# Kernel optimization log

Measured on AMD Instinct MI355X. Metric: run time of the kernel, lower is better.

The kernel has to match this reference:

```python
import jax, jax.numpy as jnp
import numpy as np

EPS_LN = 1e-5
EPS_STD = 1e-5


def _ln_dim1(z, g, b):
    # LayerNorm over channel dim (axis=1) of (B, C, T) or (B, C, 1)
    mu = z.mean(axis=1, keepdims=True)
    var = ((z - mu) ** 2).mean(axis=1, keepdims=True)
    return (z - mu) * jax.lax.rsqrt(var + EPS_LN) * g[None, :, None] + b[None, :, None]


def _stats(x, m):
    # weighted mean/std over time axis; m broadcasts over channels
    mean = (m * x).sum(axis=2)                                   # (B, C)
    std = jnp.sqrt(jnp.maximum((m * x * x).sum(axis=2) - mean ** 2, EPS_STD))
    return mean, std


def setup_inputs() -> dict:
    key = jax.random.key(0)
    ks = jax.random.split(key, 4)
    B, C, T, H = 16, 1536, 2000, 128
    x = jax.random.normal(ks[0], (B, C, T), dtype=jnp.float32)
    mask = jnp.ones((B, 1, T), dtype=jnp.float32)
    # attention MLP params (conv1x1 -> relu -> LN(dim=1) -> tanh -> conv1x1)
    w1 = jax.random.normal(ks[1], (H, 3 * C), dtype=jnp.float32) * (1.0 / np.sqrt(3 * C))
    b1 = jnp.zeros((H,), jnp.float32)
    g1 = jnp.ones((H,), jnp.float32)
    be1 = jnp.zeros((H,), jnp.float32)
    w2 = jax.random.normal(ks[2], (C, H), dtype=jnp.float32) * (1.0 / np.sqrt(H))
    b2 = jnp.zeros((C,), jnp.float32)
    g2 = jnp.ones((2 * C,), jnp.float32)
    be2 = jnp.zeros((2 * C,), jnp.float32)
    return {"x": x, "mask": mask, "w1": w1, "b1": b1, "g1": g1, "be1": be1,
            "w2": w2, "b2": b2, "g2": g2, "be2": be2}


def reference(x, mask, w1, b1, g1, be1, w2, b2, g2, be2):
    B, C, T = x.shape
    # time_attention: append masked global mean/std, broadcast over T
    total = mask.sum(axis=2, keepdims=True)                      # (B,1,1)
    mean0, std0 = _stats(x, mask / total)                        # (B,C)
    x_in = jnp.concatenate([
        x,
        jnp.broadcast_to(mean0[:, :, None], (B, C, T)),
        jnp.broadcast_to(std0[:, :, None], (B, C, T)),
    ], axis=1)                                                   # (B,3C,T)
    # attention MLP (conv1x1 == channel matmul)
    h = jnp.einsum("hc,bct->bht", w1, x_in) + b1[None, :, None]  # (B,H,T)
    h = jnp.tanh(_ln_dim1(jax.nn.relu(h), g1, be1))
    alpha = jnp.einsum("ch,bht->bct", w2, h) + b2[None, :, None]  # (B,C,T)
    # masked softmax over time
    alpha = jnp.where(mask == 0, -jnp.inf, alpha)
    alpha = jax.nn.softmax(alpha, axis=2)
    # attention-weighted stats
    mean, std = _stats(x, alpha)                                 # (B,C) each
    out = jnp.concatenate([mean, std], axis=1)[:, :, None]       # (B,2C,1)
    return _ln_dim1(out, g2, be2)
```

## Files before the change

### kernel.cpp

```cpp
#include <hip/hip_runtime.h>
#include <math.h>

constexpr int B_  = 16;
constexpr int C_  = 1536;
constexpr int T_  = 2000;
constexpr int H_  = 128;
constexpr int C3_ = 3 * C_;
constexpr int C2_ = 2 * C_;
constexpr int NT_ = 4;

typedef short bf8 __attribute__((ext_vector_type(8)));
typedef short bf4 __attribute__((ext_vector_type(4)));
typedef float f4  __attribute__((ext_vector_type(4)));

__device__ inline unsigned short f2b(float f) {
  unsigned int u = __builtin_bit_cast(unsigned int, f);
  unsigned int r = (u + 0x7FFFu + ((u >> 16) & 1u)) >> 16;
  return (unsigned short)r;
}

__global__ __launch_bounds__(256) void k_stats(
    const float* __restrict__ x, const float* __restrict__ mask,
    float* __restrict__ mean0, float* __restrict__ std0) {
  const int wave = threadIdx.x >> 6;
  const int lane = threadIdx.x & 63;
  const int row = blockIdx.x * 4 + wave;
  const int b = row / C_;
  const float4* xr = (const float4*)(x + (size_t)row * T_);
  const float4* mr = (const float4*)(mask + (size_t)b * T_);
  float sm = 0.f, s1 = 0.f, s2 = 0.f;
  for (int i = lane; i < T_ / 4; i += 64) {
    float4 xv = xr[i];
    float4 mv = mr[i];
    sm += mv.x + mv.y + mv.z + mv.w;
    s1 += mv.x * xv.x + mv.y * xv.y + mv.z * xv.z + mv.w * xv.w;
    s2 += mv.x * xv.x * xv.x + mv.y * xv.y * xv.y + mv.z * xv.z * xv.z + mv.w * xv.w * xv.w;
  }
#pragma unroll
  for (int off = 32; off; off >>= 1) {
    sm += __shfl_xor(sm, off);
    s1 += __shfl_xor(s1, off);
    s2 += __shfl_xor(s2, off);
  }
  if (lane == 0) {
    float mean = s1 / sm;
    float var = s2 / sm - mean * mean;
    mean0[row] = mean;
    std0[row] = sqrtf(fmaxf(var, 1e-5f));
  }
}

__global__ __launch_bounds__(256) void k_hconst(
    const float* __restrict__ w1, const float* __restrict__ b1,
    const float* __restrict__ mean0, const float* __restrict__ std0,
    float* __restrict__ hconst) {
  const int wave = threadIdx.x >> 6;
  const int lane = threadIdx.x & 63;
  const int idx = blockIdx.x * 4 + wave;
  const int b = idx >> 7;
  const int h = idx & (H_ - 1);
  const float* wm  = w1 + (size_t)h * C3_ + C_;
  const float* wsd = wm + C_;
  const float* mn = mean0 + b * C_;
  const float* sd = std0 + b * C_;
  float s = 0.f;
  for (int c = lane; c < C_; c += 64)
    s += wm[c] * mn[c] + wsd[c] * sd[c];
#pragma unroll
  for (int off = 32; off; off >>= 1) s += __shfl_xor(s, off);
  if (lane == 0) hconst[idx] = s + b1[h];
}

__global__ __launch_bounds__(256) void k_wl1(
    const float* __restrict__ w2, float* __restrict__ wl1) {
  const int wave = threadIdx.x >> 6;
  const int lane = threadIdx.x & 63;
  const int c = blockIdx.x * 4 + wave;
  const float* wr = w2 + (size_t)c * H_;
  float s = fabsf(wr[lane]) + fabsf(wr[lane + 64]);
#pragma unroll
  for (int off = 32; off; off >>= 1) s += __shfl_xor(s, off);
  if (lane == 0) wl1[c] = s;
}

__global__ __launch_bounds__(256) void k_gemm1_ln(
    const float* __restrict__ x, const float* __restrict__ w1,
    const float* __restrict__ hconst, const float* __restrict__ g1,
    const float* __restrict__ be1, unsigned short* __restrict__ hlnT) {
  __shared__ __align__(16) short As[2][128 * 32];
  __shared__ __align__(16) short Bs[2][64 * 32];
  const int b = blockIdx.y;
  const int t0 = blockIdx.x * 64;
  const int tid = threadIdx.x;
  const int lane = tid & 63;
  const int w = tid >> 6;
  const int l15 = lane & 15;
  const int l4 = lane >> 4;

  float4 va[4], vb[2];

  f4 acc[8];
#pragma unroll
  for (int mi = 0; mi < 8; ++mi) { f4 z = {0.f, 0.f, 0.f, 0.f}; acc[mi] = z; }

#define G1_GLOAD(K0)                                                          \
  {                                                                           \
    _Pragma("unroll")                                                         \
    for (int q = 0; q < 4; ++q) {                                             \
      int idx = q * 256 + tid;                                                \
      int row = idx >> 3, j4 = idx & 7;                                       \
      va[q] = *(const float4*)(w1 + (size_t)row * C3_ + (K0) + j4 * 4);       \
    }                                                                         \
    _Pragma("unroll")                                                         \
    for (int q = 0; q < 2; ++q) {                                             \
      int idx = q * 256 + tid;                                                \
      int k = idx >> 4, t4 = idx & 15;                                        \
      int t = t0 + t4 * 4;                                                    \
      if (t < T_)                                                             \
        vb[q] = *(const float4*)(x + ((size_t)(b * C_ + (K0) + k)) * T_ + t); \
      else                                                                    \
        vb[q] = make_float4(0.f, 0.f, 0.f, 0.f);                              \
    }                                                                         \
  }
#define G1_LSTORE(BUF)                                                        \
  {                                                                           \
    _Pragma("unroll")                                                         \
    for (int q = 0; q < 4; ++q) {                                             \
      int idx = q * 256 + tid;                                                \
      int row = idx >> 3, j4 = idx & 7;                                       \
      int slot = (j4 >> 1) ^ ((row >> 2) & 3);                                \
      bf4 p;                                                                  \
      p[0] = (short)f2b(va[q].x); p[1] = (short)f2b(va[q].y);                 \
      p[2] = (short)f2b(va[q].z); p[3] = (short)f2b(va[q].w);                 \
      *(bf4*)&As[BUF][row * 32 + slot * 8 + (j4 & 1) * 4] = p;                \
    }                                                                         \
    _Pragma("unroll")                                                         \
    for (int q = 0; q < 2; ++q) {                                             \
      int idx = q * 256 + tid;                                                \
      int k = idx >> 4, t4 = idx & 15;                                        \
      float vv[4] = {vb[q].x, vb[q].y, vb[q].z, vb[q].w};                     \
      _Pragma("unroll")                                                       \
      for (int j = 0; j < 4; ++j) {                                           \
        int row = t4 * 4 + j;                                                 \
        int slot = (k >> 3) ^ ((row >> 2) & 3);                               \
        Bs[BUF][row * 32 + slot * 8 + (k & 7)] = (short)f2b(vv[j]);           \
      }                                                                       \
    }                                                                         \
  }

  G1_GLOAD(0);
  G1_LSTORE(0);
  __syncthreads();

  const int fA = (l15 >> 2) & 3;
  const int NS = C_ / 32;
  for (int s = 0; s < NS; ++s) {
    const int cur = s & 1;
    if (s + 1 < NS) G1_GLOAD((s + 1) * 32);
    {
      const int browB = w * 16 + l15;
      bf8 bfr = *(const bf8*)&Bs[cur][browB * 32 + (l4 ^ fA) * 8];
#pragma unroll
      for (int mi = 0; mi < 8; ++mi) {
        bf8 afr = *(const bf8*)&As[cur][(mi * 16 + l15) * 32 + (l4 ^ fA) * 8];
        acc[mi] = __builtin_amdgcn_mfma_f32_16x16x32_bf16(afr, bfr, acc[mi], 0, 0, 0);
      }
    }
    if (s + 1 < NS) G1_LSTORE(cur ^ 1);
    __syncthreads();
  }

  const int t = t0 + w * 16 + l15;
  float sum = 0.f, ssq = 0.f;
#pragma unroll
  for (int mi = 0; mi < 8; ++mi) {
    float4 h4 = *(const float4*)(hconst + b * H_ + mi * 16 + l4 * 4);
    const float* hp = (const float*)&h4;
#pragma unroll
    for (int reg = 0; reg < 4; ++reg) {
      float v = fmaxf(acc[mi][reg] + hp[reg], 0.f);
      acc[mi][reg] = v;
      sum += v;
      ssq += v * v;
    }
  }
  sum += __shfl_xor(sum, 16); sum += __shfl_xor(sum, 32);
  ssq += __shfl_xor(ssq, 16); ssq += __shfl_xor(ssq, 32);
  const float mean = sum * (1.f / 128.f);
  const float rstd = rsqrtf(ssq * (1.f / 128.f) - mean * mean + 1e-5f);
  if (t < T_) {
    unsigned short* dst = hlnT + ((size_t)b * T_ + t) * H_;
#pragma unroll
    for (int mi = 0; mi < 8; ++mi) {
      float4 g4 = *(const float4*)(g1 + mi * 16 + l4 * 4);
      float4 e4 = *(const float4*)(be1 + mi * 16 + l4 * 4);
      const float* gp = (const float*)&g4;
      const float* ep = (const float*)&e4;
      bf4 p;
#pragma unroll
      for (int reg = 0; reg < 4; ++reg) {
        float o = tanhf((acc[mi][reg] - mean) * rstd * gp[reg] + ep[reg]);
        p[reg] = (short)f2b(o);
      }
      *(bf4*)&dst[mi * 16 + l4 * 4] = p;
    }
  }
}

__global__ __launch_bounds__(256) void k_gemm2_pool(
    const float* __restrict__ x, const float* __restrict__ mask,
    const float* __restrict__ w2, const unsigned short* __restrict__ hlnT,
    const float* __restrict__ wl1,
    float* __restrict__ ps0, float* __restrict__ ps1, float* __restrict__ ps2) {
  __shared__ __align__(16) short Ws[128 * 128];
  __shared__ __align__(16) short Hs[2][64 * 128];
  const int b = blockIdx.y;
  const int c0 = blockIdx.x * 128;
  const int part = blockIdx.z;
  const int tb = part * 512;
  const int te = min(tb + 512, T_);
  const int tid = threadIdx.x;
  const int lane = tid & 63;
  const int w = tid >> 6;
  const int l15 = lane & 15;
  const int l4 = lane >> 4;

#pragma unroll
  for (int q = 0; q < 16; ++q) {
    int idx = q * 256 + tid;
    int row = idx >> 5, j4 = idx & 31;
    float4 v = *(const float4*)(w2 + (size_t)(c0 + row) * H_ + j4 * 4);
    bf4 p;
    p[0] = (short)f2b(v.x); p[1] = (short)f2b(v.y);
    p[2] = (short)f2b(v.z); p[3] = (short)f2b(v.w);
    int slot = (j4 >> 1) ^ (row & 15);
    *(bf4*)&Ws[row * 128 + slot * 8 + (j4 & 1) * 4] = p;
  }

  float Mc[8];
#pragma unroll
  for (int mi = 0; mi < 2; ++mi) {
    float4 m4 = *(const float4*)(wl1 + c0 + w * 32 + mi * 16 + l4 * 4);
    Mc[mi * 4 + 0] = m4.x; Mc[mi * 4 + 1] = m4.y;
    Mc[mi * 4 + 2] = m4.z; Mc[mi * 4 + 3] = m4.w;
  }

  float s0[8], s1[8], s2[8];
#pragma unroll
  for (int r = 0; r < 8; ++r) { s0[r] = 0.f; s1[r] = 0.f; s2[r] = 0.f; }

  bf8 hreg[4];
#define G2_HLOAD(T0)                                                          \
  {                                                                           \
    _Pragma("unroll")                                                         \
    for (int q = 0; q < 4; ++q) {                                             \
      int idx = q * 256 + tid;                                                \
      int row = idx >> 4, slot = idx & 15;                                    \
      int t = (T0) + row;                                                     \
      if (t > T_ - 1) t = T_ - 1;                                             \
      hreg[q] = *(const bf8*)(hlnT + ((size_t)b * T_ + t) * H_ + slot * 8);   \
    }                                                                         \
  }
#define G2_HSTORE(BUF)                                                        \
  {                                                                           \
    _Pragma("unroll")                                                         \
    for (int q = 0; q < 4; ++q) {                                             \
      int idx = q * 256 + tid;                                                \
      int row = idx >> 4, slot = idx & 15;                                    \
      *(bf8*)&Hs[BUF][row * 128 + (slot ^ (row & 15)) * 8] = hreg[q];         \
    }                                                                         \
  }

  G2_HLOAD(tb);
  G2_HSTORE(0);
  __syncthreads();

  const int NCH = (te - tb + 63) / 64;
  for (int ch = 0; ch < NCH; ++ch) {
    const int t0 = tb + ch * 64;
    const int cur = ch & 1;
    if (ch + 1 < NCH) G2_HLOAD(t0 + 64);

    float mk[4];
    int tcol[4];
#pragma unroll
    for (int nj = 0; nj < 4; ++nj) {
      int t = t0 + nj * 16 + l15;
      tcol[nj] = (t < T_) ? t : (T_ - 1);
      mk[nj] = (t < T_) ? mask[(size_t)b * T_ + t] : 0.f;
    }
    float xv[8][4];
#pragma unroll
    for (int mi = 0; mi < 2; ++mi)
#pragma unroll
      for (int reg = 0; reg < 4; ++reg) {
        const int c = c0 + w * 32 + mi * 16 + l4 * 4 + reg;
        const float* xrow = x + ((size_t)(b * C_ + c)) * T_;
#pragma unroll
        for (int nj = 0; nj < 4; ++nj) xv[mi * 4 + reg][nj] = xrow[tcol[nj]];
      }

    f4 acc[2][4];
#pragma unroll
    for (int mi = 0; mi < 2; ++mi)
#pragma unroll
      for (int nj = 0; nj < 4; ++nj) { f4 z = {0.f, 0.f, 0.f, 0.f}; acc[mi][nj] = z; }

#pragma unroll
    for (int ks = 0; ks < 4; ++ks) {
      const int sw = (ks * 4 + l4) ^ l15;
      bf8 a0 = *(const bf8*)&Ws[(w * 32 + l15) * 128 + sw * 8];
      bf8 a1 = *(const bf8*)&Ws[(w * 32 + 16 + l15) * 128 + sw * 8];
      bf8 bb[4];
#pragma unroll
      for (int nj = 0; nj < 4; ++nj)
        bb[nj] = *(const bf8*)&Hs[cur][(nj * 16 + l15) * 128 + sw * 8];
#pragma unroll
      for (int nj = 0; nj < 4; ++nj) {
        acc[0][nj] = __builtin_amdgcn_mfma_f32_16x16x32_bf16(a0, bb[nj], acc[0][nj], 0, 0, 0);
        acc[1][nj] = __builtin_amdgcn_mfma_f32_16x16x32_bf16(a1, bb[nj], acc[1][nj], 0, 0, 0);
      }
    }

#pragma unroll
    for (int mi = 0; mi < 2; ++mi)
#pragma unroll
      for (int reg = 0; reg < 4; ++reg) {
        const int r = mi * 4 + reg;
        float a0 = s0[r], a1 = s1[r], a2 = s2[r];
#pragma unroll
        for (int nj = 0; nj < 4; ++nj) {
          float e = (mk[nj] != 0.f) ? __expf(acc[mi][nj][reg] - Mc[r]) : 0.f;
          float xvv = xv[r][nj];
          a0 += e; a1 += e * xvv; a2 += e * xvv * xvv;
        }
        s0[r] = a0; s1[r] = a1; s2[r] = a2;
      }

    if (ch + 1 < NCH) G2_HSTORE(cur ^ 1);
    __syncthreads();
  }

#pragma unroll
  for (int off = 1; off < 16; off <<= 1) {
#pragma unroll
    for (int r = 0; r < 8; ++r) {
      s0[r] += __shfl_xor(s0[r], off);
      s1[r] += __shfl_xor(s1[r], off);
      s2[r] += __shfl_xor(s2[r], off);
    }
  }
  if (l15 == 0) {
#pragma unroll
    for (int mi = 0; mi < 2; ++mi)
#pragma unroll
      for (int reg = 0; reg < 4; ++reg) {
        const int r = mi * 4 + reg;
        const int c = c0 + w * 32 + mi * 16 + l4 * 4 + reg;
        const size_t j = ((size_t)(b * NT_ + part)) * C_ + c;
        ps0[j] = s0[r]; ps1[j] = s1[r]; ps2[j] = s2[r];
      }
  }
}

__global__ __launch_bounds__(256) void k_pool_merge(
    const float* __restrict__ ps0, const float* __restrict__ ps1,
    const float* __restrict__ ps2, float* __restrict__ pooled) {
  const int idx = blockIdx.x * 256 + threadIdx.x;
  const int b = idx / C_;
  const int c = idx - b * C_;
  float s0 = 0.f, s1 = 0.f, s2 = 0.f;
#pragma unroll
  for (int p = 0; p < NT_; ++p) {
    const size_t j = ((size_t)(b * NT_ + p)) * C_ + c;
    s0 += ps0[j]; s1 += ps1[j]; s2 += ps2[j];
  }
  float mean = s1 / s0;
  float var = s2 / s0 - mean * mean;
  pooled[b * C2_ + c] = mean;
  pooled[b * C2_ + C_ + c] = sqrtf(fmaxf(var, 1e-5f));
}

__global__ __launch_bounds__(256) void k_final_ln(
    const float* __restrict__ pooled, const float* __restrict__ g2,
    const float* __restrict__ be2, float* __restrict__ out) {
  __shared__ float rs[8];
  const int b = blockIdx.x;
  const int tid = threadIdx.x;
  const int lane = tid & 63;
  const int wave = tid >> 6;
  const float* p = pooled + b * C2_;
  float s = 0.f, q = 0.f;
  for (int i = tid; i < C2_; i += 256) {
    float v = p[i];
    s += v;
    q += v * v;
  }
#pragma unroll
  for (int off = 32; off; off >>= 1) {
    s += __shfl_xor(s, off);
    q += __shfl_xor(q, off);
  }
  if (lane == 0) { rs[wave] = s; rs[4 + wave] = q; }
  __syncthreads();
  s = rs[0] + rs[1] + rs[2] + rs[3];
  q = rs[4] + rs[5] + rs[6] + rs[7];
  float mean = s * (1.f / C2_);
  float var = q * (1.f / C2_) - mean * mean;
  float rstd = rsqrtf(var + 1e-5f);
  for (int i = tid; i < C2_; i += 256)
    out[b * C2_ + i] = (p[i] - mean) * rstd * g2[i] + be2[i];
}

extern "C" void kernel_launch(void* const* d_in, const int* in_sizes, int n_in,
                              void* d_out, int out_size, void* d_ws, size_t ws_size,
                              hipStream_t stream) {
  const float* x    = (const float*)d_in[0];
  const float* mask = (const float*)d_in[1];
  const float* w1   = (const float*)d_in[2];
  const float* b1   = (const float*)d_in[3];
  const float* g1   = (const float*)d_in[4];
  const float* be1  = (const float*)d_in[5];
  const float* w2   = (const float*)d_in[6];
  const float* g2   = (const float*)d_in[8];
  const float* be2  = (const float*)d_in[9];
  float* out = (float*)d_out;

  float* ws     = (float*)d_ws;
  float* mean0  = ws;
  float* std0   = mean0 + B_ * C_;
  float* hconst = std0 + B_ * C_;
  float* pooled = hconst + B_ * H_;
  float* wl1    = pooled + B_ * C2_;
  float* ps0    = wl1 + C_;
  float* ps1    = ps0 + B_ * NT_ * C_;
  float* ps2    = ps1 + B_ * NT_ * C_;
  unsigned short* hlnT = (unsigned short*)(ps2 + B_ * NT_ * C_);

  k_stats<<<dim3(B_ * C_ / 4), dim3(256), 0, stream>>>(x, mask, mean0, std0);
  k_hconst<<<dim3(B_ * H_ / 4), dim3(256), 0, stream>>>(w1, b1, mean0, std0, hconst);
  k_wl1<<<dim3(C_ / 4), dim3(256), 0, stream>>>(w2, wl1);
  k_gemm1_ln<<<dim3((T_ + 63) / 64, B_), dim3(256), 0, stream>>>(x, w1, hconst, g1, be1, hlnT);
  k_gemm2_pool<<<dim3(C_ / 128, B_, NT_), dim3(256), 0, stream>>>(x, mask, w2, hlnT, wl1,
                                                                  ps0, ps1, ps2);
  k_pool_merge<<<dim3(B_ * C_ / 256), dim3(256), 0, stream>>>(ps0, ps1, ps2, pooled);
  k_final_ln<<<dim3(B_), dim3(256), 0, stream>>>(pooled, g2, be2, out);
}
```

Before: 165.0 us.

## Keep W2 fragments in registers, split time into more parts, merge small kernels

Removes the 32KB shared-memory W2 tile in the gemm2/pool kernel and loads each wave's A fragments straight into registers, adding a launch-bounds occupancy hint of 3 blocks. This cuts LDS use and the per-step LDS reads of A. The time axis is also split into 8 parts instead of 4 for more parallelism, at the cost of reloading W2 in more blocks and more partial sums to merge. The hconst and wl1 kernels are fused into one launch to save launch overhead.

```diff
diff --git a/kernel.cpp b/kernel.cpp
--- a/kernel.cpp
+++ b/kernel.cpp
@@ -7,7 +7,7 @@
 constexpr int H_  = 128;
 constexpr int C3_ = 3 * C_;
 constexpr int C2_ = 2 * C_;
-constexpr int NT_ = 4;
+constexpr int NT_ = 8;
 
 typedef short bf8 __attribute__((ext_vector_type(8)));
 typedef short bf4 __attribute__((ext_vector_type(4)));
@@ -50,37 +50,35 @@
   }
 }
 
-__global__ __launch_bounds__(256) void k_hconst(
+__global__ __launch_bounds__(256) void k_hconst_wl1(
     const float* __restrict__ w1, const float* __restrict__ b1,
     const float* __restrict__ mean0, const float* __restrict__ std0,
-    float* __restrict__ hconst) {
+    const float* __restrict__ w2,
+    float* __restrict__ hconst, float* __restrict__ wl1) {
   const int wave = threadIdx.x >> 6;
   const int lane = threadIdx.x & 63;
-  const int idx = blockIdx.x * 4 + wave;
-  const int b = idx >> 7;
-  const int h = idx & (H_ - 1);
-  const float* wm  = w1 + (size_t)h * C3_ + C_;
-  const float* wsd = wm + C_;
-  const float* mn = mean0 + b * C_;
-  const float* sd = std0 + b * C_;
-  float s = 0.f;
-  for (int c = lane; c < C_; c += 64)
-    s += wm[c] * mn[c] + wsd[c] * sd[c];
-#pragma unroll
-  for (int off = 32; off; off >>= 1) s += __shfl_xor(s, off);
-  if (lane == 0) hconst[idx] = s + b1[h];
-}
-
-__global__ __launch_bounds__(256) void k_wl1(
-    const float* __restrict__ w2, float* __restrict__ wl1) {
-  const int wave = threadIdx.x >> 6;
-  const int lane = threadIdx.x & 63;
-  const int c = blockIdx.x * 4 + wave;
-  const float* wr = w2 + (size_t)c * H_;
-  float s = fabsf(wr[lane]) + fabsf(wr[lane + 64]);
-#pragma unroll
-  for (int off = 32; off; off >>= 1) s += __shfl_xor(s, off);
-  if (lane == 0) wl1[c] = s;
+  if (blockIdx.x < B_ * H_ / 4) {
+    const int idx = blockIdx.x * 4 + wave;
+    const int b = idx >> 7;
+    const int h = idx & (H_ - 1);
+    const float* wm  = w1 + (size_t)h * C3_ + C_;
+    const float* wsd = wm + C_;
+    const float* mn = mean0 + b * C_;
+    const float* sd = std0 + b * C_;
+    float s = 0.f;
+    for (int c = lane; c < C_; c += 64)
+      s += wm[c] * mn[c] + wsd[c] * sd[c];
+#pragma unroll
+    for (int off = 32; off; off >>= 1) s += __shfl_xor(s, off);
+    if (lane == 0) hconst[idx] = s + b1[h];
+  } else {
+    const int c = (blockIdx.x - B_ * H_ / 4) * 4 + wave;
+    const float* wr = w2 + (size_t)c * H_;
+    float s = fabsf(wr[lane]) + fabsf(wr[lane + 64]);
+#pragma unroll
+    for (int off = 32; off; off >>= 1) s += __shfl_xor(s, off);
+    if (lane == 0) wl1[c] = s;
+  }
 }
 
 __global__ __launch_bounds__(256) void k_gemm1_ln(
@@ -207,35 +205,38 @@
   }
 }
 
-__global__ __launch_bounds__(256) void k_gemm2_pool(
+__global__ __launch_bounds__(256, 3) void k_gemm2_pool(
     const float* __restrict__ x, const float* __restrict__ mask,
     const float* __restrict__ w2, const unsigned short* __restrict__ hlnT,
     const float* __restrict__ wl1,
     float* __restrict__ ps0, float* __restrict__ ps1, float* __restrict__ ps2) {
-  __shared__ __align__(16) short Ws[128 * 128];
   __shared__ __align__(16) short Hs[2][64 * 128];
   const int b = blockIdx.y;
   const int c0 = blockIdx.x * 128;
   const int part = blockIdx.z;
-  const int tb = part * 512;
-  const int te = min(tb + 512, T_);
+  const int tb = part * 256;
+  const int te = min(tb + 256, T_);
   const int tid = threadIdx.x;
   const int lane = tid & 63;
   const int w = tid >> 6;
   const int l15 = lane & 15;
   const int l4 = lane >> 4;
 
-#pragma unroll
-  for (int q = 0; q < 16; ++q) {
-    int idx = q * 256 + tid;
-    int row = idx >> 5, j4 = idx & 31;
-    float4 v = *(const float4*)(w2 + (size_t)(c0 + row) * H_ + j4 * 4);
-    bf4 p;
-    p[0] = (short)f2b(v.x); p[1] = (short)f2b(v.y);
-    p[2] = (short)f2b(v.z); p[3] = (short)f2b(v.w);
-    int slot = (j4 >> 1) ^ (row & 15);
-    *(bf4*)&Ws[row * 128 + slot * 8 + (j4 & 1) * 4] = p;
-  }
+  bf8 af[2][4];
+#pragma unroll
+  for (int mi = 0; mi < 2; ++mi)
+#pragma unroll
+    for (int ks = 0; ks < 4; ++ks) {
+      const float* src = w2 + (size_t)(c0 + w * 32 + mi * 16 + l15) * H_ + (ks * 4 + l4) * 8;
+      float4 v0 = *(const float4*)src;
+      float4 v1 = *(const float4*)(src + 4);
+      bf8 p;
+      p[0] = (short)f2b(v0.x); p[1] = (short)f2b(v0.y);
+      p[2] = (short)f2b(v0.z); p[3] = (short)f2b(v0.w);
+      p[4] = (short)f2b(v1.x); p[5] = (short)f2b(v1.y);
+      p[6] = (short)f2b(v1.z); p[7] = (short)f2b(v1.w);
+      af[mi][ks] = p;
+    }
 
   float Mc[8];
 #pragma unroll
@@ -309,16 +310,14 @@
 #pragma unroll
     for (int ks = 0; ks < 4; ++ks) {
       const int sw = (ks * 4 + l4) ^ l15;
-      bf8 a0 = *(const bf8*)&Ws[(w * 32 + l15) * 128 + sw * 8];
-      bf8 a1 = *(const bf8*)&Ws[(w * 32 + 16 + l15) * 128 + sw * 8];
       bf8 bb[4];
 #pragma unroll
       for (int nj = 0; nj < 4; ++nj)
         bb[nj] = *(const bf8*)&Hs[cur][(nj * 16 + l15) * 128 + sw * 8];
 #pragma unroll
       for (int nj = 0; nj < 4; ++nj) {
-        acc[0][nj] = __builtin_amdgcn_mfma_f32_16x16x32_bf16(a0, bb[nj], acc[0][nj], 0, 0, 0);
-        acc[1][nj] = __builtin_amdgcn_mfma_f32_16x16x32_bf16(a1, bb[nj], acc[1][nj], 0, 0, 0);
+        acc[0][nj] = __builtin_amdgcn_mfma_f32_16x16x32_bf16(af[0][ks], bb[nj], acc[0][nj], 0, 0, 0);
+        acc[1][nj] = __builtin_amdgcn_mfma_f32_16x16x32_bf16(af[1][ks], bb[nj], acc[1][nj], 0, 0, 0);
       }
     }
 
@@ -438,8 +437,8 @@
   unsigned short* hlnT = (unsigned short*)(ps2 + B_ * NT_ * C_);
 
   k_stats<<<dim3(B_ * C_ / 4), dim3(256), 0, stream>>>(x, mask, mean0, std0);
-  k_hconst<<<dim3(B_ * H_ / 4), dim3(256), 0, stream>>>(w1, b1, mean0, std0, hconst);
-  k_wl1<<<dim3(C_ / 4), dim3(256), 0, stream>>>(w2, wl1);
+  k_hconst_wl1<<<dim3(B_ * H_ / 4 + C_ / 4), dim3(256), 0, stream>>>(
+      w1, b1, mean0, std0, w2, hconst, wl1);
   k_gemm1_ln<<<dim3((T_ + 63) / 64, B_), dim3(256), 0, stream>>>(x, w1, hconst, g1, be1, hlnT);
   k_gemm2_pool<<<dim3(C_ / 128, B_, NT_), dim3(256), 0, stream>>>(x, mask, w2, hlnT, wl1,
                                                                   ps0, ps1, ps2);
```

After: 206.4 us. 1.25x slower.
